# Optimization experiments

Hardware: AMD Instinct MI355X
Metric: run time of the kernel (lower is better)

## Reference

```python
import jax, jax.numpy as jnp
import numpy as np

N_NODES = 50000
N_EDGES = 800000
IN_CH = 128
HID = 256
N_GRAPHS = 512


def setup_inputs() -> dict:
    key = jax.random.key(0)
    ks = jax.random.split(key, 10)
    x = jax.random.normal(ks[0], (N_NODES, IN_CH), dtype=jnp.float32)
    edge_index = jax.random.randint(ks[1], (2, N_EDGES), 0, N_NODES, dtype=jnp.int32)
    batch = jnp.sort(jax.random.randint(ks[2], (N_NODES,), 0, N_GRAPHS, dtype=jnp.int32))
    # GCNConv params (glorot-ish init)
    W0 = jax.random.normal(ks[3], (IN_CH, HID), dtype=jnp.float32) / np.sqrt(IN_CH)
    b0 = jnp.zeros((HID,), dtype=jnp.float32)
    W1 = jax.random.normal(ks[4], (HID, HID), dtype=jnp.float32) / np.sqrt(HID)
    b1 = jnp.zeros((HID,), dtype=jnp.float32)
    W2 = jax.random.normal(ks[5], (HID, HID), dtype=jnp.float32) / np.sqrt(HID)
    b2 = jnp.zeros((HID,), dtype=jnp.float32)
    return {"x": x, "W0": W0, "b0": b0, "W1": W1, "b1": b1, "W2": W2, "b2": b2,
            "edge_index": edge_index, "batch": batch}


def _gcn_norm(edge_index, num_nodes):
    # PyG gcn_norm with add_self_loops=True: A_hat = A + I, norm = D^-1/2 A_hat D^-1/2
    src, dst = edge_index[0], edge_index[1]
    loop = jnp.arange(num_nodes, dtype=src.dtype)
    src = jnp.concatenate([src, loop])
    dst = jnp.concatenate([dst, loop])
    deg = jax.ops.segment_sum(jnp.ones_like(dst, dtype=jnp.float32), dst,
                              num_segments=num_nodes)
    dinv = jnp.where(deg > 0, jax.lax.rsqrt(deg), 0.0)
    norm = dinv[src] * dinv[dst]  # [E + N]
    return src, dst, norm


def _gcn_conv(x, W, b, src, dst, norm, num_nodes):
    h = x @ W                                  # [N, out]
    msg = norm[:, None] * h[src]               # gather + scale, [E+N, out]
    out = jax.ops.segment_sum(msg, dst, num_segments=num_nodes)  # scatter-add
    return out + b


def reference(x, W0, b0, W1, b1, W2, b2, edge_index, batch):
    n = x.shape[0]
    src, dst, norm = _gcn_norm(edge_index, n)  # normalization is layer-independent
    h = jax.nn.relu(_gcn_conv(x, W0, b0, src, dst, norm, n))
    h = jax.nn.relu(_gcn_conv(h, W1, b1, src, dst, norm, n))
    h = jax.nn.relu(_gcn_conv(h, W2, b2, src, dst, norm, n))
    # global_add_pool: segment-sum node features by graph id
    return jax.ops.segment_sum(h, batch, num_segments=N_GRAPHS)
```

## Files before the change

### kernel.cpp

```cpp
#include <hip/hip_runtime.h>
#include <hip/hip_fp16.h>

constexpr int NN  = 50000;
constexpr int NE  = 800000;
constexpr int CIN = 128;
constexpr int CH  = 256;
constexpr int NG  = 512;

typedef unsigned short ushort_t;
typedef unsigned int uint_t;
typedef unsigned char uchar_t;
typedef __attribute__((ext_vector_type(2))) float f32x2_t;
typedef __attribute__((ext_vector_type(2))) uint_t u32x2_t;

static __device__ __forceinline__ ushort_t f2bf(float f) {
    uint_t u = __float_as_uint(f);
    u += 0x7fffu + ((u >> 16) & 1u);
    return (ushort_t)(u >> 16);
}

static __device__ __forceinline__ float h16tof(uint_t bits) {
    return __half2float(__ushort_as_half((unsigned short)bits));
}

__global__ void conv_x_kernel(const float4* __restrict__ x, ushort4* __restrict__ xb, int n4) {
    int i = blockIdx.x * blockDim.x + threadIdx.x;
    if (i >= n4) return;
    float4 v = x[i];
    ushort4 o;
    o.x = f2bf(v.x); o.y = f2bf(v.y); o.z = f2bf(v.z); o.w = f2bf(v.w);
    xb[i] = o;
}

__global__ void conv_wt3_kernel(const float* __restrict__ W0, const float* __restrict__ W1,
                                const float* __restrict__ W2, ushort_t* __restrict__ W0t,
                                ushort_t* __restrict__ W1t, ushort_t* __restrict__ W2t) {
    int i = blockIdx.x * blockDim.x + threadIdx.x;
    if (i < 32768) {
        int k = i >> 8, n = i & 255;
        W0t[n * 128 + k] = f2bf(W0[i]);
    } else if (i < 98304) {
        int j = i - 32768;
        int k = j >> 8, n = j & 255;
        W1t[n * 256 + k] = f2bf(W1[j]);
    } else if (i < 163840) {
        int j = i - 98304;
        int k = j >> 8, n = j & 255;
        W2t[n * 256 + k] = f2bf(W2[j]);
    }
}

__global__ void count_kernel(const int* __restrict__ dst, int* __restrict__ cnt, int E) {
    int e = blockIdx.x * blockDim.x + threadIdx.x;
    if (e < E) atomicAdd(&cnt[dst[e]], 1);
}

__global__ __launch_bounds__(256) void scan_bsum_kernel(const int* __restrict__ cnt,
                                                        int* __restrict__ bsum, int n) {
    int i = blockIdx.x * 256 + threadIdx.x;
    int v = (i < n) ? ((cnt[i] + 15) & ~15) : 0;
    #pragma unroll
    for (int off = 32; off >= 1; off >>= 1) v += __shfl_xor(v, off, 64);
    __shared__ int ws[4];
    if ((threadIdx.x & 63) == 0) ws[threadIdx.x >> 6] = v;
    __syncthreads();
    if (threadIdx.x == 0) bsum[blockIdx.x] = ws[0] + ws[1] + ws[2] + ws[3];
}

__global__ __launch_bounds__(256) void scan_boff_kernel(int* __restrict__ bsum, int nb) {
    int tid = threadIdx.x, lane = tid & 63, wid = tid >> 6;
    int v = (tid < nb) ? bsum[tid] : 0;
    int s = v;
    #pragma unroll
    for (int off = 1; off < 64; off <<= 1) {
        int t = __shfl_up(s, off, 64);
        if (lane >= off) s += t;
    }
    __shared__ int wsum[4];
    if (lane == 63) wsum[wid] = s;
    __syncthreads();
    int wadd = 0;
    #pragma unroll
    for (int w = 0; w < 4; w++) if (w < wid) wadd += wsum[w];
    if (tid < nb) bsum[tid] = wadd + s - v;
}

__global__ __launch_bounds__(256) void scan_final_kernel(const int* __restrict__ cnt,
                                                         const int* __restrict__ boff,
                                                         int* __restrict__ rowptr,
                                                         float* __restrict__ dinv, int n) {
    int tid = threadIdx.x, lane = tid & 63, wid = tid >> 6;
    int i = blockIdx.x * 256 + tid;
    int c = (i < n) ? cnt[i] : 0;
    int v = (c + 15) & ~15;
    int s = v;
    #pragma unroll
    for (int off = 1; off < 64; off <<= 1) {
        int t = __shfl_up(s, off, 64);
        if (lane >= off) s += t;
    }
    __shared__ int wsum[4];
    if (lane == 63) wsum[wid] = s;
    __syncthreads();
    int wadd = boff[blockIdx.x];
    #pragma unroll
    for (int w = 0; w < 4; w++) if (w < wid) wadd += wsum[w];
    if (i < n) {
        rowptr[i] = wadd + s - v;
        dinv[i]   = rsqrtf((float)c + 1.0f);
        if (i == n - 1) rowptr[n] = wadd + s;
    }
}

__global__ void scatter_kernel(const int* __restrict__ src, const int* __restrict__ dst,
                               const int* __restrict__ rowptr, int* __restrict__ cursor,
                               const float* __restrict__ dinv, uint_t* __restrict__ epack, int E) {
    int e = blockIdx.x * blockDim.x + threadIdx.x;
    if (e >= E) return;
    int d = dst[e];
    int s = src[e];
    int p = rowptr[d] + atomicAdd(&cursor[d], 1);
    uint_t hb = (uint_t)__half_as_ushort(__float2half(dinv[s]));
    epack[p] = (uint_t)s | (hb << 16);
}

__global__ __launch_bounds__(256) void node_agg_bf16_kernel(
    const ushort_t* __restrict__ h, const int* __restrict__ rowptr,
    const int* __restrict__ degc, const uint_t* __restrict__ epack,
    const float* __restrict__ dinv, ushort_t* __restrict__ outp, int n) {
    int wave = threadIdx.x >> 6;
    int lane = threadIdx.x & 63;
    int d = blockIdx.x * 4 + wave;
    if (d >= n) return;

    int beg = __builtin_amdgcn_readfirstlane(rowptr[d]);
    int deg = __builtin_amdgcn_readfirstlane(degc[d]);
    const uint_t* hu = (const uint_t*)h;

    float a0 = 0.0f, a1 = 0.0f;
    const uint4* ep4 = (const uint4*)(epack + beg);
    uint4 e0, e1, e2, e3;
    if (deg > 0) { e0 = ep4[0]; e1 = ep4[1]; e2 = ep4[2]; e3 = ep4[3]; }
    uint4 n0 = e0, n1 = e1, n2 = e2, n3 = e3;

    for (int e = 0; e < deg; e += 16) {
        int blk = e >> 4;
        if (e + 16 < deg) {
            n0 = ep4[blk * 4 + 4]; n1 = ep4[blk * 4 + 5];
            n2 = ep4[blk * 4 + 6]; n3 = ep4[blk * 4 + 7];
        }
        uint_t eps[16] = {e0.x, e0.y, e0.z, e0.w, e1.x, e1.y, e1.z, e1.w,
                          e2.x, e2.y, e2.z, e2.w, e3.x, e3.y, e3.z, e3.w};
        int   srcs[16];
        float wts[16];
        #pragma unroll
        for (int u = 0; u < 16; u++) {
            bool a = (e + u) < deg;
            srcs[u] = a ? (int)(eps[u] & 0xffffu) : d;
            wts[u]  = a ? h16tof(eps[u] >> 16) : 0.0f;
        }
        uint_t rv[16];
        #pragma unroll
        for (int u = 0; u < 16; u++)
            rv[u] = hu[(size_t)__builtin_amdgcn_readfirstlane(srcs[u]) * 64 + lane];
        #pragma unroll
        for (int u = 0; u < 16; u++) {
            float w = wts[u];
            a0 += w * __uint_as_float(rv[u] << 16);
            a1 += w * __uint_as_float(rv[u] & 0xffff0000u);
        }
        e0 = n0; e1 = n1; e2 = n2; e3 = n3;
    }

    float dd = dinv[d];
    uint_t sv = hu[(size_t)d * 64 + lane];
    float r0 = dd * a0 + dd * dd * __uint_as_float(sv << 16);
    float r1 = dd * a1 + dd * dd * __uint_as_float(sv & 0xffff0000u);

    uint_t* o = (uint_t*)(outp + (size_t)d * CIN);
    o[lane] = (uint_t)f2bf(r0) | ((uint_t)f2bf(r1) << 16);
}

template <int MODE>
__global__ __launch_bounds__(256) void node_agg_fp8_kernel(
    const uchar_t* __restrict__ h8, const int* __restrict__ rowptr,
    const int* __restrict__ degc, const uint_t* __restrict__ epack,
    const float* __restrict__ dinv, const float* __restrict__ bias,
    const int* __restrict__ batch, void* __restrict__ out_v, int n) {
    int wave = threadIdx.x >> 6;
    int lane = threadIdx.x & 63;
    int d = blockIdx.x * 4 + wave;
    if (d >= n) return;

    int beg = __builtin_amdgcn_readfirstlane(rowptr[d]);
    int deg = __builtin_amdgcn_readfirstlane(degc[d]);
    const uint_t* hu = (const uint_t*)h8;

    float a0 = 0.0f, a1 = 0.0f, a2 = 0.0f, a3 = 0.0f;
    const uint4* ep4 = (const uint4*)(epack + beg);
    uint4 e0, e1, e2, e3;
    if (deg > 0) { e0 = ep4[0]; e1 = ep4[1]; e2 = ep4[2]; e3 = ep4[3]; }
    uint4 n0 = e0, n1 = e1, n2 = e2, n3 = e3;

    for (int e = 0; e < deg; e += 16) {
        int blk = e >> 4;
        if (e + 16 < deg) {
            n0 = ep4[blk * 4 + 4]; n1 = ep4[blk * 4 + 5];
            n2 = ep4[blk * 4 + 6]; n3 = ep4[blk * 4 + 7];
        }
        uint_t eps[16] = {e0.x, e0.y, e0.z, e0.w, e1.x, e1.y, e1.z, e1.w,
                          e2.x, e2.y, e2.z, e2.w, e3.x, e3.y, e3.z, e3.w};
        int   srcs[16];
        float wts[16];
        #pragma unroll
        for (int u = 0; u < 16; u++) {
            bool a = (e + u) < deg;
            srcs[u] = a ? (int)(eps[u] & 0xffffu) : d;
            wts[u]  = a ? h16tof(eps[u] >> 16) : 0.0f;
        }
        uint_t rv[16];
        #pragma unroll
        for (int u = 0; u < 16; u++)
            rv[u] = hu[(size_t)__builtin_amdgcn_readfirstlane(srcs[u]) * 64 + lane];
        #pragma unroll
        for (int u = 0; u < 16; u++) {
            float w = wts[u];
            f32x2_t lo = __builtin_amdgcn_cvt_pk_f32_fp8(rv[u], false);
            f32x2_t hi = __builtin_amdgcn_cvt_pk_f32_fp8(rv[u], true);
            a0 += w * lo.x;
            a1 += w * lo.y;
            a2 += w * hi.x;
            a3 += w * hi.y;
        }
        e0 = n0; e1 = n1; e2 = n2; e3 = n3;
    }

    float dd = dinv[d];
    float dd2 = dd * dd;
    uint_t sv = hu[(size_t)d * 64 + lane];
    f32x2_t slo = __builtin_amdgcn_cvt_pk_f32_fp8(sv, false);
    f32x2_t shi = __builtin_amdgcn_cvt_pk_f32_fp8(sv, true);

    float4 b4 = *(const float4*)(bias + 4 * lane);
    float r0 = fmaxf(dd * a0 + dd2 * slo.x + b4.x, 0.0f);
    float r1 = fmaxf(dd * a1 + dd2 * slo.y + b4.y, 0.0f);
    float r2 = fmaxf(dd * a2 + dd2 * shi.x + b4.z, 0.0f);
    float r3 = fmaxf(dd * a3 + dd2 * shi.y + b4.w, 0.0f);

    if constexpr (MODE == 2) {
        float* o = (float*)out_v + (size_t)batch[d] * CH + 4 * lane;
        atomicAdd(o + 0, r0);
        atomicAdd(o + 1, r1);
        atomicAdd(o + 2, r2);
        atomicAdd(o + 3, r3);
    } else {
        u32x2_t st;
        st.x = (uint_t)f2bf(r0) | ((uint_t)f2bf(r1) << 16);
        st.y = (uint_t)f2bf(r2) | ((uint_t)f2bf(r3) << 16);
        *((u32x2_t*)((ushort_t*)out_v + (size_t)d * CH) + lane) = st;
    }
}

typedef __attribute__((ext_vector_type(8))) short bf16x8;
typedef __attribute__((ext_vector_type(4))) float f32x4;

template <int MODE, int F8OUT>
__global__ __launch_bounds__(256) void gemm_bf16_kernel(
    const ushort_t* __restrict__ A, const ushort_t* __restrict__ Wt,
    const float* __restrict__ bias, void* __restrict__ Cv, int M, int K) {
    __shared__ union alignas(16) {
        ushort_t ab[2][128][40];
        uchar_t  f8[128][128];
    } smem;
    int tid = threadIdx.x;
    int row0 = blockIdx.x * 128, col0 = blockIdx.y * 128;
    int lr = tid >> 2, lq = tid & 3;
    int lane = tid & 63, wv = tid >> 6;
    int wr = (wv >> 1) * 64, wc = (wv & 1) * 64;
    int r16 = lane & 15, quad = lane >> 4;

    f32x4 acc[4][4] = {};

    for (int k0 = 0; k0 < K; k0 += 32) {
        {
            int gr0 = row0 + lr, gr1 = row0 + lr + 64;
            uint4 a0 = make_uint4(0, 0, 0, 0), a1 = make_uint4(0, 0, 0, 0);
            if (gr0 < M) a0 = *(const uint4*)(A + (size_t)gr0 * K + k0 + lq * 8);
            if (gr1 < M) a1 = *(const uint4*)(A + (size_t)gr1 * K + k0 + lq * 8);
            *(uint4*)&smem.ab[0][lr][lq * 8]      = a0;
            *(uint4*)&smem.ab[0][lr + 64][lq * 8] = a1;
            uint4 b0 = *(const uint4*)(Wt + (size_t)(col0 + lr) * K + k0 + lq * 8);
            uint4 b1 = *(const uint4*)(Wt + (size_t)(col0 + lr + 64) * K + k0 + lq * 8);
            *(uint4*)&smem.ab[1][lr][lq * 8]      = b0;
            *(uint4*)&smem.ab[1][lr + 64][lq * 8] = b1;
        }
        __syncthreads();
        bf16x8 af[4], bfr[4];
        #pragma unroll
        for (int i = 0; i < 4; i++) af[i]  = *(const bf16x8*)&smem.ab[0][wr + i * 16 + r16][quad * 8];
        #pragma unroll
        for (int j = 0; j < 4; j++) bfr[j] = *(const bf16x8*)&smem.ab[1][wc + j * 16 + r16][quad * 8];
        #pragma unroll
        for (int i = 0; i < 4; i++)
            #pragma unroll
            for (int j = 0; j < 4; j++)
                acc[i][j] = __builtin_amdgcn_mfma_f32_16x16x32_bf16(af[i], bfr[j], acc[i][j], 0, 0, 0);
        __syncthreads();
    }

    if constexpr (F8OUT) {
        #pragma unroll
        for (int j = 0; j < 4; j++) {
            int colt = wc + j * 16 + r16;
            #pragma unroll
            for (int i = 0; i < 4; i++) {
                #pragma unroll
                for (int r = 0; r < 4; r++) {
                    float v = acc[i][j][r];
                    uint_t pk = __builtin_amdgcn_cvt_pk_fp8_f32(v, v, 0u, false);
                    smem.f8[wr + i * 16 + quad * 4 + r][colt] = (uchar_t)(pk & 0xffu);
                }
            }
        }
        __syncthreads();
        uchar_t* C8 = (uchar_t*)Cv;
        #pragma unroll
        for (int k = 0; k < 4; k++) {
            int idx = k * 256 + tid;
            int r = idx >> 3, coff = (idx & 7) * 16;
            if (row0 + r < M)
                *(uint4*)(C8 + (size_t)(row0 + r) * 256 + col0 + coff) =
                    *(const uint4*)&smem.f8[r][coff];
        }
    } else {
        #pragma unroll
        for (int j = 0; j < 4; j++) {
            int colc = col0 + wc + j * 16 + r16;
            float bval = (MODE == 1) ? bias[colc] : 0.0f;
            #pragma unroll
            for (int i = 0; i < 4; i++) {
                #pragma unroll
                for (int r = 0; r < 4; r++) {
                    int row = row0 + wr + i * 16 + quad * 4 + r;
                    if (row < M) {
                        float v = acc[i][j][r];
                        if (MODE == 1) v = fmaxf(v + bval, 0.0f);
                        ((ushort_t*)Cv)[(size_t)row * 256 + colc] = f2bf(v);
                    }
                }
            }
        }
    }
}

extern "C" void kernel_launch(void* const* d_in, const int* in_sizes, int n_in,
                              void* d_out, int out_size, void* d_ws, size_t ws_size,
                              hipStream_t stream) {
    const float* x   = (const float*)d_in[0];
    const float* W0  = (const float*)d_in[1];
    const float* b0  = (const float*)d_in[2];
    const float* W1  = (const float*)d_in[3];
    const float* b1  = (const float*)d_in[4];
    const float* W2  = (const float*)d_in[5];
    const float* b2  = (const float*)d_in[6];
    const int*   ei  = (const int*)d_in[7];
    const int*   src = ei;
    const int*   dst = ei + NE;
    const int*   batch = (const int*)d_in[8];
    float* out = (float*)d_out;

    char* ws = (char*)d_ws;
    ushort_t* P1  = (ushort_t*)ws;
    ushort_t* G0  = (ushort_t*)(ws + 25600000ull);
    uchar_t*  F8  = (uchar_t*) (ws + 38400000ull);
    ushort_t* xbf = (ushort_t*)(ws + 51200000ull);
    ushort_t* W0t = (ushort_t*)(ws + 64000000ull);
    ushort_t* W1t = (ushort_t*)(ws + 64065536ull);
    ushort_t* W2t = (ushort_t*)(ws + 64196608ull);
    float*    dinv   = (float*)(ws + 64327680ull);
    int*      rowptr = (int*)  (ws + 64527680ull);
    int*      cnt    = (int*)  (ws + 64727808ull);
    uint_t*   epack  = (uint_t*)(ws + 64927808ull);
    int*      bsum   = (int*)  (ws + 71327808ull);
    int*      cursor = (int*)ws;

    const int scanBlocks = (NN + 255) / 256;
    const int nodeBlocks = (NN + 3) / 4;
    const dim3 ggrid((NN + 127) / 128, 2);

    conv_x_kernel<<<(NN * CIN / 4 + 255) / 256, 256, 0, stream>>>((const float4*)x, (ushort4*)xbf, NN * CIN / 4);
    conv_wt3_kernel<<<640, 256, 0, stream>>>(W0, W1, W2, W0t, W1t, W2t);

    hipMemsetAsync(cnt, 0, (size_t)NN * 4, stream);
    count_kernel<<<(NE + 255) / 256, 256, 0, stream>>>(dst, cnt, NE);
    scan_bsum_kernel<<<scanBlocks, 256, 0, stream>>>(cnt, bsum, NN);
    scan_boff_kernel<<<1, 256, 0, stream>>>(bsum, scanBlocks);
    scan_final_kernel<<<scanBlocks, 256, 0, stream>>>(cnt, bsum, rowptr, dinv, NN);
    hipMemsetAsync(cursor, 0, (size_t)NN * 4, stream);
    scatter_kernel<<<(NE + 255) / 256, 256, 0, stream>>>(src, dst, rowptr, cursor, dinv, epack, NE);

    node_agg_bf16_kernel<<<nodeBlocks, 256, 0, stream>>>(xbf, rowptr, cnt, epack, dinv, G0, NN);
    gemm_bf16_kernel<1, 0><<<ggrid, 256, 0, stream>>>(G0, W0t, b0, P1, NN, CIN);

    gemm_bf16_kernel<0, 1><<<ggrid, 256, 0, stream>>>(P1, W1t, nullptr, F8, NN, CH);
    node_agg_fp8_kernel<1><<<nodeBlocks, 256, 0, stream>>>(F8, rowptr, cnt, epack, dinv, b1, nullptr, P1, NN);

    gemm_bf16_kernel<0, 1><<<ggrid, 256, 0, stream>>>(P1, W2t, nullptr, F8, NN, CH);
    hipMemsetAsync(out, 0, (size_t)NG * CH * 4, stream);
    node_agg_fp8_kernel<2><<<nodeBlocks, 256, 0, stream>>>(F8, rowptr, cnt, epack, dinv, b2, batch, out, NN);
}
```

Measured before the change: 492.4 us.

## Drop input conversion pass, fold memsets into kernels, shrink edge padding to 8

```diff
diff --git a/kernel.cpp b/kernel.cpp
--- a/kernel.cpp
+++ b/kernel.cpp
@@ -23,19 +23,12 @@
     return __half2float(__ushort_as_half((unsigned short)bits));
 }
 
-__global__ void conv_x_kernel(const float4* __restrict__ x, ushort4* __restrict__ xb, int n4) {
-    int i = blockIdx.x * blockDim.x + threadIdx.x;
-    if (i >= n4) return;
-    float4 v = x[i];
-    ushort4 o;
-    o.x = f2bf(v.x); o.y = f2bf(v.y); o.z = f2bf(v.z); o.w = f2bf(v.w);
-    xb[i] = o;
-}
-
 __global__ void conv_wt3_kernel(const float* __restrict__ W0, const float* __restrict__ W1,
                                 const float* __restrict__ W2, ushort_t* __restrict__ W0t,
-                                ushort_t* __restrict__ W1t, ushort_t* __restrict__ W2t) {
+                                ushort_t* __restrict__ W1t, ushort_t* __restrict__ W2t,
+                                int* __restrict__ cnt) {
     int i = blockIdx.x * blockDim.x + threadIdx.x;
+    if (i < NN) cnt[i] = 0;
     if (i < 32768) {
         int k = i >> 8, n = i & 255;
         W0t[n * 128 + k] = f2bf(W0[i]);
@@ -58,7 +51,7 @@
 __global__ __launch_bounds__(256) void scan_bsum_kernel(const int* __restrict__ cnt,
                                                         int* __restrict__ bsum, int n) {
     int i = blockIdx.x * 256 + threadIdx.x;
-    int v = (i < n) ? ((cnt[i] + 15) & ~15) : 0;
+    int v = (i < n) ? ((cnt[i] + 7) & ~7) : 0;
     #pragma unroll
     for (int off = 32; off >= 1; off >>= 1) v += __shfl_xor(v, off, 64);
     __shared__ int ws[4];
@@ -88,11 +81,12 @@
 __global__ __launch_bounds__(256) void scan_final_kernel(const int* __restrict__ cnt,
                                                          const int* __restrict__ boff,
                                                          int* __restrict__ rowptr,
-                                                         float* __restrict__ dinv, int n) {
+                                                         float* __restrict__ dinv,
+                                                         int* __restrict__ cursor, int n) {
     int tid = threadIdx.x, lane = tid & 63, wid = tid >> 6;
     int i = blockIdx.x * 256 + tid;
     int c = (i < n) ? cnt[i] : 0;
-    int v = (c + 15) & ~15;
+    int v = (c + 7) & ~7;
     int s = v;
     #pragma unroll
     for (int off = 1; off < 64; off <<= 1) {
@@ -108,6 +102,7 @@
     if (i < n) {
         rowptr[i] = wadd + s - v;
         dinv[i]   = rsqrtf((float)c + 1.0f);
+        cursor[i] = 0;
         if (i == n - 1) rowptr[n] = wadd + s;
     }
 }
@@ -124,8 +119,8 @@
     epack[p] = (uint_t)s | (hb << 16);
 }
 
-__global__ __launch_bounds__(256) void node_agg_bf16_kernel(
-    const ushort_t* __restrict__ h, const int* __restrict__ rowptr,
+__global__ __launch_bounds__(256) void node_agg_f32_kernel(
+    const float* __restrict__ x, const int* __restrict__ rowptr,
     const int* __restrict__ degc, const uint_t* __restrict__ epack,
     const float* __restrict__ dinv, ushort_t* __restrict__ outp, int n) {
     int wave = threadIdx.x >> 6;
@@ -135,47 +130,44 @@
 
     int beg = __builtin_amdgcn_readfirstlane(rowptr[d]);
     int deg = __builtin_amdgcn_readfirstlane(degc[d]);
-    const uint_t* hu = (const uint_t*)h;
 
     float a0 = 0.0f, a1 = 0.0f;
     const uint4* ep4 = (const uint4*)(epack + beg);
-    uint4 e0, e1, e2, e3;
-    if (deg > 0) { e0 = ep4[0]; e1 = ep4[1]; e2 = ep4[2]; e3 = ep4[3]; }
-    uint4 n0 = e0, n1 = e1, n2 = e2, n3 = e3;
-
-    for (int e = 0; e < deg; e += 16) {
-        int blk = e >> 4;
-        if (e + 16 < deg) {
-            n0 = ep4[blk * 4 + 4]; n1 = ep4[blk * 4 + 5];
-            n2 = ep4[blk * 4 + 6]; n3 = ep4[blk * 4 + 7];
-        }
-        uint_t eps[16] = {e0.x, e0.y, e0.z, e0.w, e1.x, e1.y, e1.z, e1.w,
-                          e2.x, e2.y, e2.z, e2.w, e3.x, e3.y, e3.z, e3.w};
-        int   srcs[16];
-        float wts[16];
-        #pragma unroll
-        for (int u = 0; u < 16; u++) {
+    uint4 ea, eb, na, nb;
+    if (deg > 0) { ea = ep4[0]; eb = ep4[1]; }
+    na = ea; nb = eb;
+
+    for (int e = 0; e < deg; e += 8) {
+        int blk = e >> 3;
+        if (e + 8 < deg) { na = ep4[blk * 2 + 2]; nb = ep4[blk * 2 + 3]; }
+        uint_t eps[8] = {ea.x, ea.y, ea.z, ea.w, eb.x, eb.y, eb.z, eb.w};
+        int   srcs[8];
+        float wts[8];
+        #pragma unroll
+        for (int u = 0; u < 8; u++) {
             bool a = (e + u) < deg;
             srcs[u] = a ? (int)(eps[u] & 0xffffu) : d;
             wts[u]  = a ? h16tof(eps[u] >> 16) : 0.0f;
         }
-        uint_t rv[16];
-        #pragma unroll
-        for (int u = 0; u < 16; u++)
-            rv[u] = hu[(size_t)__builtin_amdgcn_readfirstlane(srcs[u]) * 64 + lane];
-        #pragma unroll
-        for (int u = 0; u < 16; u++) {
+        float2 rv[8];
+        #pragma unroll
+        for (int u = 0; u < 8; u++) {
+            const float2* row = (const float2*)(x + (size_t)__builtin_amdgcn_readfirstlane(srcs[u]) * CIN);
+            rv[u] = row[lane];
+        }
+        #pragma unroll
+        for (int u = 0; u < 8; u++) {
             float w = wts[u];
-            a0 += w * __uint_as_float(rv[u] << 16);
-            a1 += w * __uint_as_float(rv[u] & 0xffff0000u);
-        }
-        e0 = n0; e1 = n1; e2 = n2; e3 = n3;
+            a0 += w * rv[u].x;
+            a1 += w * rv[u].y;
+        }
+        ea = na; eb = nb;
     }
 
     float dd = dinv[d];
-    uint_t sv = hu[(size_t)d * 64 + lane];
-    float r0 = dd * a0 + dd * dd * __uint_as_float(sv << 16);
-    float r1 = dd * a1 + dd * dd * __uint_as_float(sv & 0xffff0000u);
+    float2 sv = ((const float2*)(x + (size_t)d * CIN))[lane];
+    float r0 = dd * a0 + dd * dd * sv.x;
+    float r1 = dd * a1 + dd * dd * sv.y;
 
     uint_t* o = (uint_t*)(outp + (size_t)d * CIN);
     o[lane] = (uint_t)f2bf(r0) | ((uint_t)f2bf(r1) << 16);
@@ -198,32 +190,28 @@
 
     float a0 = 0.0f, a1 = 0.0f, a2 = 0.0f, a3 = 0.0f;
     const uint4* ep4 = (const uint4*)(epack + beg);
-    uint4 e0, e1, e2, e3;
-    if (deg > 0) { e0 = ep4[0]; e1 = ep4[1]; e2 = ep4[2]; e3 = ep4[3]; }
-    uint4 n0 = e0, n1 = e1, n2 = e2, n3 = e3;
-
-    for (int e = 0; e < deg; e += 16) {
-        int blk = e >> 4;
-        if (e + 16 < deg) {
-            n0 = ep4[blk * 4 + 4]; n1 = ep4[blk * 4 + 5];
-            n2 = ep4[blk * 4 + 6]; n3 = ep4[blk * 4 + 7];
-        }
-        uint_t eps[16] = {e0.x, e0.y, e0.z, e0.w, e1.x, e1.y, e1.z, e1.w,
-                          e2.x, e2.y, e2.z, e2.w, e3.x, e3.y, e3.z, e3.w};
-        int   srcs[16];
-        float wts[16];
-        #pragma unroll
-        for (int u = 0; u < 16; u++) {
+    uint4 ea, eb, na, nb;
+    if (deg > 0) { ea = ep4[0]; eb = ep4[1]; }
+    na = ea; nb = eb;
+
+    for (int e = 0; e < deg; e += 8) {
+        int blk = e >> 3;
+        if (e + 8 < deg) { na = ep4[blk * 2 + 2]; nb = ep4[blk * 2 + 3]; }
+        uint_t eps[8] = {ea.x, ea.y, ea.z, ea.w, eb.x, eb.y, eb.z, eb.w};
+        int   srcs[8];
+        float wts[8];
+        #pragma unroll
+        for (int u = 0; u < 8; u++) {
             bool a = (e + u) < deg;
             srcs[u] = a ? (int)(eps[u] & 0xffffu) : d;
             wts[u]  = a ? h16tof(eps[u] >> 16) : 0.0f;
         }
-        uint_t rv[16];
-        #pragma unroll
-        for (int u = 0; u < 16; u++)
+        uint_t rv[8];
+        #pragma unroll
+        for (int u = 0; u < 8; u++)
             rv[u] = hu[(size_t)__builtin_amdgcn_readfirstlane(srcs[u]) * 64 + lane];
         #pragma unroll
-        for (int u = 0; u < 16; u++) {
+        for (int u = 0; u < 8; u++) {
             float w = wts[u];
             f32x2_t lo = __builtin_amdgcn_cvt_pk_f32_fp8(rv[u], false);
             f32x2_t hi = __builtin_amdgcn_cvt_pk_f32_fp8(rv[u], true);
@@ -232,7 +220,7 @@
             a2 += w * hi.x;
             a3 += w * hi.y;
         }
-        e0 = n0; e1 = n1; e2 = n2; e3 = n3;
+        ea = na; eb = nb;
     }
 
     float dd = dinv[d];
@@ -373,7 +361,6 @@
     ushort_t* P1  = (ushort_t*)ws;
     ushort_t* G0  = (ushort_t*)(ws + 25600000ull);
     uchar_t*  F8  = (uchar_t*) (ws + 38400000ull);
-    ushort_t* xbf = (ushort_t*)(ws + 51200000ull);
     ushort_t* W0t = (ushort_t*)(ws + 64000000ull);
     ushort_t* W1t = (ushort_t*)(ws + 64065536ull);
     ushort_t* W2t = (ushort_t*)(ws + 64196608ull);
@@ -388,24 +375,21 @@
     const int nodeBlocks = (NN + 3) / 4;
     const dim3 ggrid((NN + 127) / 128, 2);
 
-    conv_x_kernel<<<(NN * CIN / 4 + 255) / 256, 256, 0, stream>>>((const float4*)x, (ushort4*)xbf, NN * CIN / 4);
-    conv_wt3_kernel<<<640, 256, 0, stream>>>(W0, W1, W2, W0t, W1t, W2t);
-
-    hipMemsetAsync(cnt, 0, (size_t)NN * 4, stream);
+    conv_wt3_kernel<<<640, 256, 0, stream>>>(W0, W1, W2, W0t, W1t, W2t, cnt);
+
     count_kernel<<<(NE + 255) / 256, 256, 0, stream>>>(dst, cnt, NE);
     scan_bsum_kernel<<<scanBlocks, 256, 0, stream>>>(cnt, bsum, NN);
     scan_boff_kernel<<<1, 256, 0, stream>>>(bsum, scanBlocks);
-    scan_final_kernel<<<scanBlocks, 256, 0, stream>>>(cnt, bsum, rowptr, dinv, NN);
-    hipMemsetAsync(cursor, 0, (size_t)NN * 4, stream);
+    scan_final_kernel<<<scanBlocks, 256, 0, stream>>>(cnt, bsum, rowptr, dinv, cursor, NN);
     scatter_kernel<<<(NE + 255) / 256, 256, 0, stream>>>(src, dst, rowptr, cursor, dinv, epack, NE);
-
-    node_agg_bf16_kernel<<<nodeBlocks, 256, 0, stream>>>(xbf, rowptr, cnt, epack, dinv, G0, NN);
+    hipMemsetAsync(out, 0, (size_t)NG * CH * 4, stream);
+
+    node_agg_f32_kernel<<<nodeBlocks, 256, 0, stream>>>(x, rowptr, cnt, epack, dinv, G0, NN);
     gemm_bf16_kernel<1, 0><<<ggrid, 256, 0, stream>>>(G0, W0t, b0, P1, NN, CIN);
 
     gemm_bf16_kernel<0, 1><<<ggrid, 256, 0, stream>>>(P1, W1t, nullptr, F8, NN, CH);
     node_agg_fp8_kernel<1><<<nodeBlocks, 256, 0, stream>>>(F8, rowptr, cnt, epack, dinv, b1, nullptr, P1, NN);
 
     gemm_bf16_kernel<0, 1><<<ggrid, 256, 0, stream>>>(P1, W2t, nullptr, F8, NN, CH);
-    hipMemsetAsync(out, 0, (size_t)NG * CH * 4, stream);
     node_agg_fp8_kernel<2><<<nodeBlocks, 256, 0, stream>>>(F8, rowptr, cnt, epack, dinv, b2, batch, out, NN);
 }
```

New measurement: 498.3 us. No clear change (+1.2%).
